# Performance work log

Measured on AMD Instinct MI355X. Metric: run time of the kernel, lower is better.

Reference implementation:

```python
import jax, jax.numpy as jnp
import numpy as np

B, N, C, H, R = 16, 1024, 768, 12, 16
HD = C // H
SCALE = HD ** -0.5


def setup_inputs() -> dict:
    key = jax.random.key(0)
    ks = jax.random.split(key, 13)
    f = lambda k, shape, s=0.02: jax.random.normal(k, shape, dtype=jnp.float32) * s
    return {
        "x": jax.random.normal(ks[0], (B, N, C), dtype=jnp.float32),
        "W_qkv": f(ks[1], (3 * C, C)),
        "b_qkv": f(ks[2], (3 * C,)),
        "W_proj": f(ks[3], (C, C)),
        "b_proj": f(ks[4], (C,)),
        "A_q": f(ks[5], (R, C)),
        "B_q": f(ks[6], (C, R)),
        "A_k": f(ks[7], (R, C)),
        "B_k": f(ks[8], (C, R)),
        "A_v": f(ks[9], (R, C)),
        "B_v": f(ks[10], (C, R)),
        "A_o": f(ks[11], (R, C)),
        "B_o": f(ks[12], (C, R)),
    }


def _lora(x, A, Bu):
    # Adapter with no norm/act/bias, scaling=1.0: low-rank x @ A^T @ B^T
    return (x @ A.T) @ Bu.T


def _heads(t):
    # [B, N, C] -> [B, H, N, HD]
    return t.reshape(B, N, H, HD).transpose(0, 2, 1, 3)


def reference(x, W_qkv, b_qkv, W_proj, b_proj, A_q, B_q, A_k, B_k, A_v, B_v, A_o, B_o):
    qkv = x @ W_qkv.T + b_qkv                    # [B, N, 3C]
    qkv = qkv.reshape(B, N, 3, H, HD).transpose(2, 0, 3, 1, 4)  # [3, B, H, N, HD]
    q, k, v = qkv[0], qkv[1], qkv[2]
    q = q + _heads(_lora(x, A_q, B_q))
    k = k + _heads(_lora(x, A_k, B_k))
    v = v + _heads(_lora(x, A_v, B_v))
    attn = jnp.einsum("bhnd,bhmd->bhnm", q, k) * SCALE
    attn = jax.nn.softmax(attn, axis=-1)
    out = jnp.einsum("bhnm,bhmd->bhnd", attn, v)  # [B, H, N, HD]
    out = out.transpose(0, 2, 1, 3).reshape(B, N, C)
    out = out @ W_proj.T + b_proj
    out = out + _lora(out, A_o, B_o)
    return out
```

## Files before the change

kernel.cpp:

```cpp
#include <hip/hip_runtime.h>
#include <cmath>


#define DEVI __device__ __forceinline__

typedef float f32x4 __attribute__((ext_vector_type(4)));
typedef short s16x8 __attribute__((ext_vector_type(8)));
typedef short s16x4 __attribute__((ext_vector_type(4)));
typedef __bf16 b16x8 __attribute__((ext_vector_type(8)));
typedef unsigned int u32x4 __attribute__((ext_vector_type(4)));
typedef unsigned int u32x2 __attribute__((ext_vector_type(2)));

static constexpr int MTOT = 16384;
static constexpr int C = 768;
static constexpr int N3 = 2304;

DEVI unsigned short f2bf(float x) {
  unsigned int u = __builtin_bit_cast(unsigned int, x);
  return (unsigned short)((u + 0x7FFFu + ((u >> 16) & 1u)) >> 16);
}

DEVI f32x4 mfma16(s16x8 a, s16x8 b, f32x4 c) {
  return __builtin_amdgcn_mfma_f32_16x16x32_bf16(
      __builtin_bit_cast(b16x8, a), __builtin_bit_cast(b16x8, b), c, 0, 0, 0);
}

#if __has_builtin(__builtin_amdgcn_mfma_f32_16x16x16bf16_1k)
#define HAVE_MFMA_X16 1
DEVI f32x4 mfma16h(s16x4 a, s16x4 b, f32x4 c) {
  return __builtin_amdgcn_mfma_f32_16x16x16bf16_1k(a, b, c, 0, 0, 0);
}
#else
#define HAVE_MFMA_X16 0
DEVI f32x4 mfma16h(s16x4 a, s16x4 b, f32x4 c) {
  u32x2 au = __builtin_bit_cast(u32x2, a), bu = __builtin_bit_cast(u32x2, b);
  u32x4 a8 = {au[0], au[1], 0u, 0u}, b8 = {bu[0], bu[1], 0u, 0u};
  return mfma16(__builtin_bit_cast(s16x8, a8), __builtin_bit_cast(s16x8, b8), c);
}
#endif

DEVI void async16(const void* g, void* l) {
  __builtin_amdgcn_global_load_lds(
      (__attribute__((address_space(1))) void*)g,
      (__attribute__((address_space(3))) void*)l, 16, 0, 0);
}


__global__ __launch_bounds__(256) void k_prep_x(const float* __restrict__ x,
                                                unsigned short* __restrict__ xb) {
  int idx = (blockIdx.x * 256 + threadIdx.x) * 4;
  float4 v = *(const float4*)(x + idx);
  uint2 p;
  p.x = (unsigned int)f2bf(v.x) | ((unsigned int)f2bf(v.y) << 16);
  p.y = (unsigned int)f2bf(v.z) | ((unsigned int)f2bf(v.w) << 16);
  *(uint2*)(xb + idx) = p;
}

__global__ __launch_bounds__(256) void k_prep_wqkv(
    const float* __restrict__ W, const float* __restrict__ Aq,
    const float* __restrict__ Bq, const float* __restrict__ Ak,
    const float* __restrict__ Bk, const float* __restrict__ Av,
    const float* __restrict__ Bv, unsigned short* __restrict__ out) {
  int idx = blockIdx.x * 256 + threadIdx.x;
  int n = idx / 768, c = idx - n * 768;
  int s = n / 768, co = n - s * 768;
  const float* A = (s == 0) ? Aq : (s == 1) ? Ak : Av;
  const float* Bm = (s == 0) ? Bq : (s == 1) ? Bk : Bv;
  float acc = W[idx];
#pragma unroll
  for (int r = 0; r < 16; ++r) acc += Bm[co * 16 + r] * A[r * 768 + c];
  out[idx] = f2bf(acc);
}

__global__ __launch_bounds__(256) void k_prep_M(const float* __restrict__ Ao,
                                                const float* __restrict__ Wp,
                                                float* __restrict__ M) {
  __shared__ float red[4][64];
  const int r = blockIdx.x, j0 = blockIdx.y * 64;
  const int jl = threadIdx.x & 63, cs = threadIdx.x >> 6;
  float acc = 0.f;
#pragma unroll 4
  for (int c = cs * 192; c < cs * 192 + 192; ++c)
    acc += Ao[r * 768 + c] * Wp[c * 768 + j0 + jl];
  red[cs][jl] = acc;
  __syncthreads();
  if (cs == 0)
    M[r * 768 + j0 + jl] = red[0][jl] + red[1][jl] + red[2][jl] + red[3][jl];
}

__global__ __launch_bounds__(256) void k_prep_wpe(const float* __restrict__ Wp,
                                                  const float* __restrict__ Bo,
                                                  const float* __restrict__ M,
                                                  unsigned short* __restrict__ out) {
  int idx = blockIdx.x * 256 + threadIdx.x;
  int n = idx / 768, j = idx - n * 768;
  float acc = Wp[idx];
#pragma unroll
  for (int r = 0; r < 16; ++r) acc += Bo[n * 16 + r] * M[r * 768 + j];
  out[idx] = f2bf(acc);
}

__global__ __launch_bounds__(256) void k_prep_beff(const float* __restrict__ bp,
                                                   const float* __restrict__ Ao,
                                                   const float* __restrict__ Bo,
                                                   float* __restrict__ beff) {
  __shared__ float red[256];
  __shared__ float bv[16];
  const int t = threadIdx.x;
  const int r = t >> 4, cs = t & 15;
  float a = 0.f;
#pragma unroll 4
  for (int c = cs * 48; c < cs * 48 + 48; ++c) a += Ao[r * 768 + c] * bp[c];
  red[t] = a;
  __syncthreads();
  if (cs == 0) {
    float s = 0.f;
#pragma unroll
    for (int k = 0; k < 16; ++k) s += red[r * 16 + k];
    bv[r] = s;
  }
  __syncthreads();
#pragma unroll
  for (int it = 0; it < 3; ++it) {
    const int n = it * 256 + t;
    float acc = bp[n];
#pragma unroll
    for (int r2 = 0; r2 < 16; ++r2) acc += Bo[n * 16 + r2] * bv[r2];
    beff[n] = acc;
  }
}


template <bool SWAP>
__global__ __launch_bounds__(256) void k_gemm_qkv_t(
    const unsigned short* __restrict__ A, const unsigned short* __restrict__ Bw,
    const float* __restrict__ bias, int nblk0, unsigned short* __restrict__ qb,
    unsigned short* __restrict__ kb, unsigned short* __restrict__ vtb) {
  __shared__ short la[2][128 * 32];
  __shared__ short lb[2][128 * 32];
  const int t = threadIdx.x;
  const int w = t >> 6, l = t & 63;
  const int i = l & 15, qd = l >> 4;
  const int wm = w >> 1, wn = w & 1;
  const int mblk = blockIdx.x, nblk = nblk0 + blockIdx.y;

  const unsigned short* Ab = A + (size_t)(mblk * 128) * 768;
  const unsigned short* Bb = Bw + (size_t)(nblk * 128) * 768;
  const int sr = l >> 2;
  const int sc = (l & 3) * 8;

  auto stage = [&](int bufn, int kb_) {
    const int k0 = kb_ * 32;
#pragma unroll
    for (int j = 0; j < 2; ++j) {
      const int row = w * 32 + j * 16 + sr;
      async16(Ab + row * 768 + k0 + sc, &la[bufn][(w * 32 + j * 16) * 32]);
      async16(Bb + row * 768 + k0 + sc, &lb[bufn][(w * 32 + j * 16) * 32]);
    }
  };

  stage(0, 0);

  f32x4 acc[4][4] = {};

  for (int kb_ = 0; kb_ < 24; ++kb_) {
    const int buf = kb_ & 1;
    __syncthreads();
    if (kb_ < 23) stage(buf ^ 1, kb_ + 1);
    s16x8 af[4], bf[4];
#pragma unroll
    for (int mi = 0; mi < 4; ++mi)
      af[mi] = *(const s16x8*)&la[buf][(wm * 64 + mi * 16 + i) * 32 + qd * 8];
#pragma unroll
    for (int ni = 0; ni < 4; ++ni)
      bf[ni] = *(const s16x8*)&lb[buf][(wn * 64 + ni * 16 + i) * 32 + qd * 8];
#pragma unroll
    for (int mi = 0; mi < 4; ++mi)
#pragma unroll
      for (int ni = 0; ni < 4; ++ni) {
        if constexpr (SWAP)
          acc[mi][ni] = mfma16(bf[ni], af[mi], acc[mi][ni]);
        else
          acc[mi][ni] = mfma16(af[mi], bf[ni], acc[mi][ni]);
      }
  }

  const float c1 = 0.18033688011112042f;
  if constexpr (SWAP) {
#pragma unroll
    for (int ni = 0; ni < 4; ++ni) {
      const int n0 = nblk * 128 + wn * 64 + ni * 16 + qd * 4;
      const int s = n0 / 768;
      const int nrel = n0 - s * 768;
      const int h = nrel >> 6, d0 = nrel & 63;
      const float4 bv4 = *(const float4*)(bias + n0);
      unsigned short* dst = (s == 0) ? qb : kb;
      const float scl = (s == 0) ? c1 : 1.0f;
#pragma unroll
      for (int mi = 0; mi < 4; ++mi) {
        const int m = mblk * 128 + wm * 64 + mi * 16 + i;
        const int b = m >> 10, pos = m & 1023;
        uint2 pk;
        pk.x = (unsigned int)f2bf((acc[mi][ni][0] + bv4.x) * scl) |
               ((unsigned int)f2bf((acc[mi][ni][1] + bv4.y) * scl) << 16);
        pk.y = (unsigned int)f2bf((acc[mi][ni][2] + bv4.z) * scl) |
               ((unsigned int)f2bf((acc[mi][ni][3] + bv4.w) * scl) << 16);
        *(uint2*)&dst[(size_t)((b * 12 + h) * 1024 + pos) * 64 + d0] = pk;
      }
    }
  } else {
#pragma unroll
    for (int ni = 0; ni < 4; ++ni) {
      const int n = nblk * 128 + wn * 64 + ni * 16 + i;
      const int nrel = n - 1536;
      const int h = nrel >> 6, d = nrel & 63;
      const float bvv = bias[n];
#pragma unroll
      for (int mi = 0; mi < 4; ++mi) {
        const int m0 = mblk * 128 + wm * 64 + mi * 16 + qd * 4;
        const int b = m0 >> 10, pos0 = m0 & 1023;
        uint2 pk;
        pk.x = (unsigned int)f2bf(acc[mi][ni][0] + bvv) |
               ((unsigned int)f2bf(acc[mi][ni][1] + bvv) << 16);
        pk.y = (unsigned int)f2bf(acc[mi][ni][2] + bvv) |
               ((unsigned int)f2bf(acc[mi][ni][3] + bvv) << 16);
        *(uint2*)&vtb[(size_t)((b * 12 + h) * 64 + d) * 1024 + pos0] = pk;
      }
    }
  }
}


__global__ __launch_bounds__(256, 4) void k_attn(
    const unsigned short* __restrict__ qg, const unsigned short* __restrict__ kg,
    const unsigned short* __restrict__ vtg, unsigned short* __restrict__ og) {
  __shared__ short k_lds[2][64 * 64];
  __shared__ short vt_lds[2][64 * 64];

  const int t = threadIdx.x;
  const int w = t >> 6, l = t & 63;
  const int i = l & 15, qd = l >> 4;
  const int ix7 = l & 7;
  const int bh = blockIdx.x;
  const int qblk = blockIdx.y;
  const int h = bh % 12, b = bh / 12;

  const unsigned short* Qg = qg + (size_t)(bh * 1024 + qblk * 128) * 64;
  const unsigned short* Kg = kg + (size_t)bh * 1024 * 64;
  const unsigned short* Vtg = vtg + (size_t)bh * 64 * 1024;

  const int srl = l >> 3;
  const int sgc = (l & 7) ^ srl;

  s16x8 qf[2][2];
#pragma unroll
  for (int nq = 0; nq < 2; ++nq)
#pragma unroll
    for (int k0 = 0; k0 < 2; ++k0)
      qf[nq][k0] =
          *(const s16x8*)(Qg + (w * 32 + nq * 16 + i) * 64 + k0 * 32 + qd * 8);

  auto stage = [&](int bufn, int tkv) {
#pragma unroll
    for (int it = 0; it < 2; ++it) {
      const int rbase = it * 32 + w * 8;
      async16(Kg + (size_t)(tkv * 64 + rbase + srl) * 64 + sgc * 8,
              &k_lds[bufn][rbase * 64]);
      async16(Vtg + (size_t)(rbase + srl) * 1024 + tkv * 64 + sgc * 8,
              &vt_lds[bufn][rbase * 64]);
    }
  };

  stage(0, 0);

  f32x4 oacc[2][4] = {};
  f32x4 lacc[2] = {};
  const u32x2 ones_u = {0x3F803F80u, 0x3F803F80u};
  const s16x4 ones4 = __builtin_bit_cast(s16x4, ones_u);

  for (int tkv = 0; tkv < 16; ++tkv) {
    const int buf = tkv & 1;
    __syncthreads();
    if (tkv < 15) stage(buf ^ 1, tkv + 1);

#pragma unroll
    for (int mi = 0; mi < 4; ++mi) {
      f32x4 st[2] = {};
#pragma unroll
      for (int k0 = 0; k0 < 2; ++k0) {
        const s16x8 kf = *(const s16x8*)&k_lds[buf][(mi * 16 + i) * 64 +
                                                    (((k0 * 4 + qd) ^ ix7) * 8)];
        st[0] = mfma16(kf, qf[0][k0], st[0]);
        st[1] = mfma16(kf, qf[1][k0], st[1]);
      }

      s16x4 pa4[2];
#pragma unroll
      for (int mq = 0; mq < 2; ++mq) {
        unsigned int u0 = __builtin_bit_cast(
            unsigned int, __builtin_amdgcn_exp2f(st[mq][0]));
        unsigned int u1 = __builtin_bit_cast(
            unsigned int, __builtin_amdgcn_exp2f(st[mq][1]));
        unsigned int u2 = __builtin_bit_cast(
            unsigned int, __builtin_amdgcn_exp2f(st[mq][2]));
        unsigned int u3 = __builtin_bit_cast(
            unsigned int, __builtin_amdgcn_exp2f(st[mq][3]));
        u32x2 p;
        p[0] = __builtin_amdgcn_perm(u1, u0, 0x07060302u);
        p[1] = __builtin_amdgcn_perm(u3, u2, 0x07060302u);
        pa4[mq] = __builtin_bit_cast(s16x4, p);
      }

#pragma unroll
      for (int nd = 0; nd < 4; ++nd) {
        const uint2 v = *(const uint2*)&vt_lds[buf][(nd * 16 + i) * 64 +
                                                    ((((mi * 2 + (qd >> 1)) ^ ix7) * 8) +
                                                     (qd & 1) * 4)];
        const s16x4 vf = __builtin_bit_cast(s16x4, v);
        oacc[0][nd] = mfma16h(pa4[0], vf, oacc[0][nd]);
        oacc[1][nd] = mfma16h(pa4[1], vf, oacc[1][nd]);
      }
      lacc[0] = mfma16h(pa4[0], ones4, lacc[0]);
      lacc[1] = mfma16h(pa4[1], ones4, lacc[1]);
    }
  }

  const int orow0 = qblk * 128 + w * 32;
#pragma unroll
  for (int mq = 0; mq < 2; ++mq) {
    float linv[4];
#pragma unroll
    for (int r = 0; r < 4; ++r) linv[r] = 1.0f / lacc[mq][r];
#pragma unroll
    for (int nd = 0; nd < 4; ++nd)
#pragma unroll
      for (int r = 0; r < 4; ++r) {
        const int pos = orow0 + mq * 16 + qd * 4 + r;
        const int d = nd * 16 + i;
        og[(size_t)(b * 1024 + pos) * 768 + h * 64 + d] =
            f2bf(oacc[mq][nd][r] * linv[r]);
      }
  }
}


__global__ __launch_bounds__(256) void k_gemm_proj(
    const unsigned short* __restrict__ A, const unsigned short* __restrict__ Bw,
    const float* __restrict__ bias, float* __restrict__ out) {
  __shared__ short la[2][128 * 32];
  __shared__ short lb[2][128 * 32];
  const int t = threadIdx.x;
  const int w = t >> 6, l = t & 63;
  const int i = l & 15, qd = l >> 4;
  const int wm = w >> 1, wn = w & 1;
  const int mblk = blockIdx.x, nblk = blockIdx.y;

  const unsigned short* Ab = A + (size_t)(mblk * 128) * 768;
  const unsigned short* Bb = Bw + (size_t)(nblk * 128) * 768;
  const int sr = l >> 2;
  const int sc = (l & 3) * 8;

  auto stage = [&](int bufn, int kb_) {
    const int k0 = kb_ * 32;
#pragma unroll
    for (int j = 0; j < 2; ++j) {
      const int row = w * 32 + j * 16 + sr;
      async16(Ab + row * 768 + k0 + sc, &la[bufn][(w * 32 + j * 16) * 32]);
      async16(Bb + row * 768 + k0 + sc, &lb[bufn][(w * 32 + j * 16) * 32]);
    }
  };

  stage(0, 0);

  f32x4 acc[4][4] = {};

  for (int kb_ = 0; kb_ < 24; ++kb_) {
    const int buf = kb_ & 1;
    __syncthreads();
    if (kb_ < 23) stage(buf ^ 1, kb_ + 1);
    s16x8 af[4], bf[4];
#pragma unroll
    for (int mi = 0; mi < 4; ++mi)
      af[mi] = *(const s16x8*)&la[buf][(wm * 64 + mi * 16 + i) * 32 + qd * 8];
#pragma unroll
    for (int ni = 0; ni < 4; ++ni)
      bf[ni] = *(const s16x8*)&lb[buf][(wn * 64 + ni * 16 + i) * 32 + qd * 8];
#pragma unroll
    for (int mi = 0; mi < 4; ++mi)
#pragma unroll
      for (int ni = 0; ni < 4; ++ni)
        acc[mi][ni] = mfma16(bf[ni], af[mi], acc[mi][ni]);
  }

#pragma unroll
  for (int ni = 0; ni < 4; ++ni) {
    const int n0 = nblk * 128 + wn * 64 + ni * 16 + qd * 4;
    const float4 bv4 = *(const float4*)(bias + n0);
#pragma unroll
    for (int mi = 0; mi < 4; ++mi) {
      const int m = mblk * 128 + wm * 64 + mi * 16 + i;
      float4 o;
      o.x = acc[mi][ni][0] + bv4.x;
      o.y = acc[mi][ni][1] + bv4.y;
      o.z = acc[mi][ni][2] + bv4.z;
      o.w = acc[mi][ni][3] + bv4.w;
      *(float4*)&out[(size_t)m * 768 + n0] = o;
    }
  }
}


extern "C" void kernel_launch(void* const* d_in, const int* in_sizes, int n_in,
                              void* d_out, int out_size, void* d_ws, size_t ws_size,
                              hipStream_t stream) {
  const float* x = (const float*)d_in[0];
  const float* Wqkv = (const float*)d_in[1];
  const float* bqkv = (const float*)d_in[2];
  const float* Wp = (const float*)d_in[3];
  const float* bp = (const float*)d_in[4];
  const float* Aq = (const float*)d_in[5];
  const float* Bq = (const float*)d_in[6];
  const float* Ak = (const float*)d_in[7];
  const float* Bk = (const float*)d_in[8];
  const float* Av = (const float*)d_in[9];
  const float* Bv = (const float*)d_in[10];
  const float* Ao = (const float*)d_in[11];
  const float* Bo = (const float*)d_in[12];
  float* out = (float*)d_out;

  unsigned short* xb = (unsigned short*)d_ws;
  unsigned short* wqkvb = xb + (size_t)MTOT * C;
  unsigned short* wpeb = wqkvb + (size_t)N3 * C;
  unsigned short* qb = wpeb + (size_t)C * C;
  unsigned short* kb = qb + (size_t)MTOT * C;
  unsigned short* vtb = kb + (size_t)MTOT * C;
  float* Mbuf = (float*)(vtb + (size_t)MTOT * C);
  float* beff = Mbuf + 16 * 768;
  unsigned short* ob = xb;

  k_prep_x<<<12288, 256, 0, stream>>>(x, xb);
  k_prep_wqkv<<<6912, 256, 0, stream>>>(Wqkv, Aq, Bq, Ak, Bk, Av, Bv, wqkvb);
  k_prep_M<<<dim3(16, 12), 256, 0, stream>>>(Ao, Wp, Mbuf);
  k_prep_wpe<<<2304, 256, 0, stream>>>(Wp, Bo, Mbuf, wpeb);
  k_prep_beff<<<1, 256, 0, stream>>>(bp, Ao, Bo, beff);

  k_gemm_qkv_t<true><<<dim3(128, 12), 256, 0, stream>>>(xb, wqkvb, bqkv, 0,
                                                        qb, kb, vtb);
  k_gemm_qkv_t<false><<<dim3(128, 6), 256, 0, stream>>>(xb, wqkvb, bqkv, 12,
                                                        qb, kb, vtb);
  k_attn<<<dim3(192, 8), 256, 0, stream>>>(qb, kb, vtb, ob);
  k_gemm_proj<<<dim3(128, 6), 256, 0, stream>>>(ob, wpeb, beff, out);
}
```

Baseline: 356.4 us.

## Switch attention kernel to 32x32x16 bf16 MFMA tiles

Rewrites the attention inner loop to use 32x32x16 bf16 MFMA instructions instead of 16x16x32 for QK^T and 16x16x16 for PV. Each wave now computes a 32-query by 32-key score tile per instruction, and the exp2'd probabilities feed the PV MFMA directly as full 8-element operands. This is meant to cut MFMA instruction count and the per-instruction issue overhead, and to replace the half-width 16x16x16 PV MFMAs. In exchange it uses larger accumulators and more registers, and changes the LDS read and output index mapping, which risks errors.

```diff
diff --git a/kernel.cpp b/kernel.cpp
--- a/kernel.cpp
+++ b/kernel.cpp
@@ -5,11 +5,10 @@
 #define DEVI __device__ __forceinline__
 
 typedef float f32x4 __attribute__((ext_vector_type(4)));
+typedef float f32x16 __attribute__((ext_vector_type(16)));
 typedef short s16x8 __attribute__((ext_vector_type(8)));
-typedef short s16x4 __attribute__((ext_vector_type(4)));
 typedef __bf16 b16x8 __attribute__((ext_vector_type(8)));
 typedef unsigned int u32x4 __attribute__((ext_vector_type(4)));
-typedef unsigned int u32x2 __attribute__((ext_vector_type(2)));
 
 static constexpr int MTOT = 16384;
 static constexpr int C = 768;
@@ -25,19 +24,10 @@
       __builtin_bit_cast(b16x8, a), __builtin_bit_cast(b16x8, b), c, 0, 0, 0);
 }
 
-#if __has_builtin(__builtin_amdgcn_mfma_f32_16x16x16bf16_1k)
-#define HAVE_MFMA_X16 1
-DEVI f32x4 mfma16h(s16x4 a, s16x4 b, f32x4 c) {
-  return __builtin_amdgcn_mfma_f32_16x16x16bf16_1k(a, b, c, 0, 0, 0);
-}
-#else
-#define HAVE_MFMA_X16 0
-DEVI f32x4 mfma16h(s16x4 a, s16x4 b, f32x4 c) {
-  u32x2 au = __builtin_bit_cast(u32x2, a), bu = __builtin_bit_cast(u32x2, b);
-  u32x4 a8 = {au[0], au[1], 0u, 0u}, b8 = {bu[0], bu[1], 0u, 0u};
-  return mfma16(__builtin_bit_cast(s16x8, a8), __builtin_bit_cast(s16x8, b8), c);
-}
-#endif
+DEVI f32x16 mfma32(s16x8 a, s16x8 b, f32x16 c) {
+  return __builtin_amdgcn_mfma_f32_32x32x16_bf16(
+      __builtin_bit_cast(b16x8, a), __builtin_bit_cast(b16x8, b), c, 0, 0, 0);
+}
 
 DEVI void async16(const void* g, void* l) {
   __builtin_amdgcn_global_load_lds(
@@ -239,8 +229,8 @@
 
   const int t = threadIdx.x;
   const int w = t >> 6, l = t & 63;
-  const int i = l & 15, qd = l >> 4;
-  const int ix7 = l & 7;
+  const int lc = l & 31;
+  const int hi = l >> 5;
   const int bh = blockIdx.x;
   const int qblk = blockIdx.y;
   const int h = bh % 12, b = bh / 12;
@@ -252,13 +242,10 @@
   const int srl = l >> 3;
   const int sgc = (l & 7) ^ srl;
 
-  s16x8 qf[2][2];
-#pragma unroll
-  for (int nq = 0; nq < 2; ++nq)
-#pragma unroll
-    for (int k0 = 0; k0 < 2; ++k0)
-      qf[nq][k0] =
-          *(const s16x8*)(Qg + (w * 32 + nq * 16 + i) * 64 + k0 * 32 + qd * 8);
+  s16x8 qf[4];
+#pragma unroll
+  for (int kc = 0; kc < 4; ++kc)
+    qf[kc] = *(const s16x8*)(Qg + (w * 32 + lc) * 64 + kc * 16 + hi * 8);
 
   auto stage = [&](int bufn, int tkv) {
 #pragma unroll
@@ -273,10 +260,10 @@
 
   stage(0, 0);
 
-  f32x4 oacc[2][4] = {};
-  f32x4 lacc[2] = {};
-  const u32x2 ones_u = {0x3F803F80u, 0x3F803F80u};
-  const s16x4 ones4 = __builtin_bit_cast(s16x4, ones_u);
+  f32x16 oacc[2] = {};
+  f32x16 lacc = {};
+  const u32x4 ones_u = {0x3F803F80u, 0x3F803F80u, 0x3F803F80u, 0x3F803F80u};
+  const s16x8 ones8 = __builtin_bit_cast(s16x8, ones_u);
 
   for (int tkv = 0; tkv < 16; ++tkv) {
     const int buf = tkv & 1;
@@ -284,63 +271,71 @@
     if (tkv < 15) stage(buf ^ 1, tkv + 1);
 
 #pragma unroll
-    for (int mi = 0; mi < 4; ++mi) {
-      f32x4 st[2] = {};
-#pragma unroll
-      for (int k0 = 0; k0 < 2; ++k0) {
-        const s16x8 kf = *(const s16x8*)&k_lds[buf][(mi * 16 + i) * 64 +
-                                                    (((k0 * 4 + qd) ^ ix7) * 8)];
-        st[0] = mfma16(kf, qf[0][k0], st[0]);
-        st[1] = mfma16(kf, qf[1][k0], st[1]);
-      }
-
-      s16x4 pa4[2];
-#pragma unroll
-      for (int mq = 0; mq < 2; ++mq) {
-        unsigned int u0 = __builtin_bit_cast(
-            unsigned int, __builtin_amdgcn_exp2f(st[mq][0]));
-        unsigned int u1 = __builtin_bit_cast(
-            unsigned int, __builtin_amdgcn_exp2f(st[mq][1]));
-        unsigned int u2 = __builtin_bit_cast(
-            unsigned int, __builtin_amdgcn_exp2f(st[mq][2]));
-        unsigned int u3 = __builtin_bit_cast(
-            unsigned int, __builtin_amdgcn_exp2f(st[mq][3]));
-        u32x2 p;
-        p[0] = __builtin_amdgcn_perm(u1, u0, 0x07060302u);
-        p[1] = __builtin_amdgcn_perm(u3, u2, 0x07060302u);
-        pa4[mq] = __builtin_bit_cast(s16x4, p);
-      }
-
-#pragma unroll
-      for (int nd = 0; nd < 4; ++nd) {
-        const uint2 v = *(const uint2*)&vt_lds[buf][(nd * 16 + i) * 64 +
-                                                    ((((mi * 2 + (qd >> 1)) ^ ix7) * 8) +
-                                                     (qd & 1) * 4)];
-        const s16x4 vf = __builtin_bit_cast(s16x4, v);
-        oacc[0][nd] = mfma16h(pa4[0], vf, oacc[0][nd]);
-        oacc[1][nd] = mfma16h(pa4[1], vf, oacc[1][nd]);
-      }
-      lacc[0] = mfma16h(pa4[0], ones4, lacc[0]);
-      lacc[1] = mfma16h(pa4[1], ones4, lacc[1]);
-    }
-  }
-
+    for (int pg = 0; pg < 2; ++pg) {
+      const int krow = pg * 32 + lc;
+      f32x16 st = {};
+#pragma unroll
+      for (int kc = 0; kc < 4; ++kc) {
+        const s16x8 ka = *(const s16x8*)&k_lds[buf][krow * 64 +
+                                                    (((kc * 2 + hi) ^ (krow & 7)) * 8)];
+        st = mfma32(ka, qf[kc], st);
+      }
+      unsigned pk[4][2];
+#pragma unroll
+      for (int q = 0; q < 4; ++q) {
+        unsigned u0 = __builtin_bit_cast(unsigned int,
+                                         __builtin_amdgcn_exp2f(st[4 * q + 0]));
+        unsigned u1 = __builtin_bit_cast(unsigned int,
+                                         __builtin_amdgcn_exp2f(st[4 * q + 1]));
+        unsigned u2 = __builtin_bit_cast(unsigned int,
+                                         __builtin_amdgcn_exp2f(st[4 * q + 2]));
+        unsigned u3 = __builtin_bit_cast(unsigned int,
+                                         __builtin_amdgcn_exp2f(st[4 * q + 3]));
+        pk[q][0] = __builtin_amdgcn_perm(u1, u0, 0x07060302u);
+        pk[q][1] = __builtin_amdgcn_perm(u3, u2, 0x07060302u);
+      }
+#pragma unroll
+      for (int m = 0; m < 2; ++m) {
+        const int mi = pg * 2 + m;
+        u32x4 fa;
+        fa[0] = pk[2 * m][0];
+        fa[1] = pk[2 * m][1];
+        fa[2] = pk[2 * m + 1][0];
+        fa[3] = pk[2 * m + 1][1];
+        const s16x8 paf = __builtin_bit_cast(s16x8, fa);
+#pragma unroll
+        for (int nd = 0; nd < 2; ++nd) {
+          const int vrow = nd * 32 + lc;
+          const uint2 vlo = *(const uint2*)&vt_lds[buf][vrow * 64 +
+                                                        (((2 * mi) ^ (vrow & 7)) * 8) +
+                                                        4 * hi];
+          const uint2 vhi = *(const uint2*)&vt_lds[buf][vrow * 64 +
+                                                        (((2 * mi + 1) ^ (vrow & 7)) * 8) +
+                                                        4 * hi];
+          u32x4 vbu;
+          vbu[0] = vlo.x;
+          vbu[1] = vlo.y;
+          vbu[2] = vhi.x;
+          vbu[3] = vhi.y;
+          oacc[nd] = mfma32(paf, __builtin_bit_cast(s16x8, vbu), oacc[nd]);
+        }
+        lacc = mfma32(paf, ones8, lacc);
+      }
+    }
+  }
+
+  float linv[16];
+#pragma unroll
+  for (int r = 0; r < 16; ++r) linv[r] = 1.0f / lacc[r];
   const int orow0 = qblk * 128 + w * 32;
 #pragma unroll
-  for (int mq = 0; mq < 2; ++mq) {
-    float linv[4];
-#pragma unroll
-    for (int r = 0; r < 4; ++r) linv[r] = 1.0f / lacc[mq][r];
-#pragma unroll
-    for (int nd = 0; nd < 4; ++nd)
-#pragma unroll
-      for (int r = 0; r < 4; ++r) {
-        const int pos = orow0 + mq * 16 + qd * 4 + r;
-        const int d = nd * 16 + i;
-        og[(size_t)(b * 1024 + pos) * 768 + h * 64 + d] =
-            f2bf(oacc[mq][nd][r] * linv[r]);
-      }
-  }
+  for (int nd = 0; nd < 2; ++nd)
+#pragma unroll
+    for (int r = 0; r < 16; ++r) {
+      const int pos = orow0 + (r & 3) + 8 * (r >> 2) + 4 * hi;
+      const int d = nd * 32 + lc;
+      og[(size_t)(b * 1024 + pos) * 768 + h * 64 + d] = f2bf(oacc[nd][r] * linv[r]);
+    }
 }
 
 
```

Result: slower. 373.7 us (+4.9%).
